# Kernel tuning notes

Hardware: AMD Instinct MI355X
Metric: run time of the kernel (lower is better)

Reference implementation:

```python
import jax, jax.numpy as jnp
import numpy as np

N_NODES = 50000


def _gcn_conv(x, src, dst, W, b, n_nodes):
    # x: [N, Fin] -> h: [N, Fout]; GCN: D^-1/2 (A+I) D^-1/2 (x W) + b
    h = x @ W
    deg = jax.ops.segment_sum(jnp.ones_like(dst, dtype=h.dtype), dst,
                              num_segments=n_nodes)
    dinv = jax.lax.rsqrt(jnp.maximum(deg, 1.0))
    norm = dinv[src] * dinv[dst]                      # [E]
    msg = h[src] * norm[:, None]                      # [E, Fout] gather
    agg = jax.ops.segment_sum(msg, dst, num_segments=n_nodes)  # scatter-add
    return agg + b


def setup_inputs() -> dict:
    key = jax.random.key(0)
    k0, k1, k2, k3 = jax.random.split(key, 4)
    N, E, F_IN, H, C = N_NODES, 800000, 128, 128, 16
    x = jax.random.normal(k0, (N, F_IN), dtype=jnp.float32)
    edge_index = jax.random.randint(k1, (2, E), 0, N, dtype=jnp.int64)
    W1 = jax.random.normal(k2, (F_IN, H), dtype=jnp.float32) / np.sqrt(F_IN)
    b1 = jnp.zeros((H,), dtype=jnp.float32)
    W2 = jax.random.normal(k3, (H, C), dtype=jnp.float32) / np.sqrt(H)
    b2 = jnp.zeros((C,), dtype=jnp.float32)
    return {"x": x, "edge_index": edge_index, "W1": W1, "b1": b1,
            "W2": W2, "b2": b2}


def reference(x, edge_index, W1, b1, W2, b2):
    n = x.shape[0]
    # add self-loops (shared by both conv layers)
    loops = jnp.arange(n, dtype=edge_index.dtype)
    src = jnp.concatenate([edge_index[0], loops])
    dst = jnp.concatenate([edge_index[1], loops])
    h = _gcn_conv(x, src, dst, W1, b1, n)
    h = jax.nn.relu(h)
    # dropout p=0.5 is identity in eval mode
    h = _gcn_conv(h, src, dst, W2, b2, n)
    return jax.nn.log_softmax(h, axis=1)
```

## Files before the change

kernel.cpp:

```cpp
#include <hip/hip_runtime.h>
#include <hip/hip_fp16.h>
#include <math.h>


#define NBUCKET_SHIFT 8
#define BIN_CHUNK 4096
#define PAD_SLOP (7 << NBUCKET_SHIFT)
#define CAP  5120
#define CCAP (CAP + PAD_SLOP)

typedef __bf16 bf16x8 __attribute__((ext_vector_type(8)));
typedef float  f32x4  __attribute__((ext_vector_type(4)));
typedef float  f32x2  __attribute__((ext_vector_type(2)));

__device__ __forceinline__ unsigned short pack_bf16(float f) {
    unsigned u = __float_as_uint(f);
    return (unsigned short)((u + 0x7fffu + ((u >> 16) & 1u)) >> 16);
}

__device__ __forceinline__ float unpack_w(unsigned u) {
    return __half2float(__ushort_as_half((unsigned short)(u >> 16)));
}

__device__ __forceinline__ void acc_fp8x16_fma(f32x2* a, uint4 v, float w) {
    f32x2 ww; ww.x = w; ww.y = w;
    a[0] += __builtin_amdgcn_cvt_pk_f32_fp8(v.x, false) * ww;
    a[1] += __builtin_amdgcn_cvt_pk_f32_fp8(v.x, true)  * ww;
    a[2] += __builtin_amdgcn_cvt_pk_f32_fp8(v.y, false) * ww;
    a[3] += __builtin_amdgcn_cvt_pk_f32_fp8(v.y, true)  * ww;
    a[4] += __builtin_amdgcn_cvt_pk_f32_fp8(v.z, false) * ww;
    a[5] += __builtin_amdgcn_cvt_pk_f32_fp8(v.z, true)  * ww;
    a[6] += __builtin_amdgcn_cvt_pk_f32_fp8(v.w, false) * ww;
    a[7] += __builtin_amdgcn_cvt_pk_f32_fp8(v.w, true)  * ww;
}

__device__ __forceinline__ void acc_fp16x8(f32x2* a, uint4 v) {
    float2 f;
    f = __half22float2(*(const __half2*)&v.x); a[0] += *(f32x2*)&f;
    f = __half22float2(*(const __half2*)&v.y); a[1] += *(f32x2*)&f;
    f = __half22float2(*(const __half2*)&v.z); a[2] += *(f32x2*)&f;
    f = __half22float2(*(const __half2*)&v.w); a[3] += *(f32x2*)&f;
}

union K1Smem {
    struct { unsigned spair[BIN_CHUNK]; int lcnt[256]; int lbase[256]; } b;
    unsigned short wtp[16384];
    float outb[4][16 * 132];
};

__global__ __launch_bounds__(256)
void bin_gemm1_kernel(const int* __restrict__ src, const int* __restrict__ dst,
                      int* __restrict__ bcur, unsigned* __restrict__ pairs,
                      int* __restrict__ deg, int E, int nbuckets, int nbins,
                      const float* __restrict__ x, const float* __restrict__ W1,
                      unsigned* __restrict__ h1b, int N) {
    __shared__ K1Smem sm;
    const int blk = blockIdx.x;
    const int tid = threadIdx.x;

    if (blk < nbins) {
        const int e0 = blk * BIN_CHUNK;
        const int cnt = min(BIN_CHUNK, E - e0);
        sm.b.lcnt[tid] = 0;
        __syncthreads();
        for (int i = tid; i < cnt; i += 256) {
            unsigned s = (unsigned)src[e0 + i], d = (unsigned)dst[e0 + i];
            sm.b.spair[i] = (d >> NBUCKET_SHIFT) << 24 | (d & 255u) << 16 | s;
            atomicAdd(&sm.b.lcnt[d >> NBUCKET_SHIFT], 1);
            atomicAdd(&deg[d], 1);
        }
        __syncthreads();
        if (tid < nbuckets) {
            int c = sm.b.lcnt[tid];
            sm.b.lbase[tid] = (c > 0) ? atomicAdd(&bcur[tid], c) : 0;
            sm.b.lcnt[tid] = 0;
        }
        __syncthreads();
        for (int i = tid; i < cnt; i += 256) {
            unsigned p = sm.b.spair[i];
            int b = (int)(p >> 24);
            int off = atomicAdd(&sm.b.lcnt[b], 1);
            pairs[b * CAP + sm.b.lbase[b] + off] = p;
        }
        return;
    }

    const int gblk = blk - nbins;
    const int wave = tid >> 6, lane = tid & 63;
    const int q = lane >> 4, m = lane & 15;
    const int row0 = gblk * 64 + wave * 16;
    const int row = row0 + m;
    const int rowc = (row < N) ? row : (N - 1);

    for (int it = tid; it < 16384; it += 256) {
        int k = it >> 7, n = it & 127;
        int t = n >> 4, mm = n & 15;
        int ks = k >> 5;
        int lane2 = (((k & 31) >> 3) << 4) | mm;
        int j = k & 7;
        sm.wtp[(t * 4 + ks) * 512 + lane2 * 8 + j] = pack_bf16(W1[it]);
    }
    __syncthreads();

    f32x4 acc[8];
#pragma unroll
    for (int t = 0; t < 8; t++) acc[t] = (f32x4)0.0f;

#pragma unroll
    for (int ks = 0; ks < 4; ks++) {
        const float4* xp = (const float4*)(x + (size_t)rowc * 128 + ks * 32 + q * 8);
        float4 f0 = xp[0], f1 = xp[1];
        float fv[8] = {f0.x, f0.y, f0.z, f0.w, f1.x, f1.y, f1.z, f1.w};
        bf16x8 ah;
#pragma unroll
        for (int j = 0; j < 8; j++) ah[j] = (__bf16)fv[j];
#pragma unroll
        for (int t = 0; t < 8; t++) {
            bf16x8 b = *(const bf16x8*)(sm.wtp + (size_t)(t * 4 + ks) * 512 + lane * 8);
            acc[t] = __builtin_amdgcn_mfma_f32_16x16x32_bf16(ah, b, acc[t], 0, 0, 0);
        }
    }
    __syncthreads();

#pragma unroll
    for (int t = 0; t < 8; t++)
#pragma unroll
        for (int r = 0; r < 4; r++)
            sm.outb[wave][(q * 4 + r) * 132 + t * 16 + m] = acc[t][r];
    __syncthreads();

    const int r2 = lane >> 2, j = lane & 3;
    const int orow = row0 + r2;
    if (orow < N) {
        const float* lrow = &sm.outb[wave][r2 * 132];
#pragma unroll
        for (int s = 0; s < 4; s++) {
            float4 a = *(const float4*)(lrow + s * 32 + j * 8);
            float4 b = *(const float4*)(lrow + s * 32 + j * 8 + 4);
            unsigned lo = __builtin_amdgcn_cvt_pk_fp8_f32(a.x, a.y, 0, false);
            lo = __builtin_amdgcn_cvt_pk_fp8_f32(a.z, a.w, lo, true);
            unsigned hi = __builtin_amdgcn_cvt_pk_fp8_f32(b.x, b.y, 0, false);
            hi = __builtin_amdgcn_cvt_pk_fp8_f32(b.z, b.w, hi, true);
            ((uint2*)h1b)[((size_t)(s >> 1) * (N + 1) + orow) * 8 + (s & 1) * 4 + j]
                = make_uint2(lo, hi);
        }
    }
}

__global__ __launch_bounds__(256)
void bucket_build_kernel(const int* __restrict__ bcur, const unsigned* __restrict__ pairs,
                         const int* __restrict__ deg,
                         int* __restrict__ rowptr, int* __restrict__ rowcnt,
                         float* __restrict__ dinv, unsigned* __restrict__ colsrc,
                         unsigned* __restrict__ h1b, int N, int nbuckets) {
    __shared__ int cnt[256];
    __shared__ int sm[256];
    const int tid = threadIdx.x;
    const int blk = blockIdx.x;
    const int nb0 = blk << NBUCKET_SHIFT;

    if (blk == 0) {
        if (tid < 16) h1b[((size_t)0 * (N + 1) + N) * 16 + tid] = 0u;
        else if (tid < 32) h1b[((size_t)1 * (N + 1) + N) * 16 + (tid - 16)] = 0u;
        else if (tid == 32) dinv[N] = 0.0f;
    }

    const int lo = blk * CAP;
    const int hi = lo + bcur[blk];

    int node = nb0 + tid;
    int v = (node < N) ? deg[node] : 0;
    int pdeg = (v + 7) & ~7;
    sm[tid] = pdeg;
    __syncthreads();
#pragma unroll
    for (int off = 1; off < 256; off <<= 1) {
        int u = (tid >= off) ? sm[tid - off] : 0;
        __syncthreads();
        sm[tid] += u;
        __syncthreads();
    }
    int pexcl = sm[tid] - pdeg;
    const int start = blk * CCAP + pexcl;
    if (node < N) {
        rowptr[node] = start;
        rowcnt[node] = pdeg;
        dinv[node] = rsqrtf((float)v + 1.0f);
    }
    __syncthreads();
    cnt[tid] = start;
    __syncthreads();
    for (int i = lo + tid; i < hi; i += 256) {
        unsigned p = pairs[i];
        unsigned s = p & 0xffffu;
        int pos = atomicAdd(&cnt[(int)(p >> 16) & 255], 1);
        float w = rsqrtf((float)deg[s] + 1.0f);
        unsigned w16 = (unsigned)__half_as_ushort(__float2half_rn(w));
        colsrc[pos] = s | (w16 << 16);
    }
    for (int p = start + v; p < start + pdeg; ++p)
        colsrc[p] = (unsigned)N;
}

__global__ __launch_bounds__(256)
void l1_fused_kernel(const int* __restrict__ rowptr, const int* __restrict__ rowcnt,
                     const unsigned* __restrict__ colsrc,
                     const float* __restrict__ dinv, const unsigned* __restrict__ h1b,
                     const float* __restrict__ b1, const float* __restrict__ W2,
                     float* __restrict__ h2acc, int N) {
    __shared__ float rows[4][4][68];
    __shared__ float w2s[64 * 16];
    const int tid = threadIdx.x;
    const int wave = tid >> 6, lane = tid & 63;
    const int c = lane & 3;
    const int g = (lane >> 2) & 3;
    const int n = lane >> 4;
    const int p = blockIdx.x & 1;
    const int d = (blockIdx.x >> 1) * 16 + wave * 4 + n;

    for (int i = tid; i < 256; i += 256)
        ((float4*)w2s)[i] = ((const float4*)W2)[p * 256 + i];

    const uint4* hq = (const uint4*)h1b + (size_t)p * (N + 1) * 4;

    if (d < N) {
        const float dvd = dinv[d];
        f32x2 a[8];
#pragma unroll
        for (int j = 0; j < 8; j++) a[j] = (f32x2)0.0f;

        if (g == 0)
            acc_fp8x16_fma(a, hq[(size_t)d * 4 + c], dvd);

        int i = rowptr[d];
        const int end = i + rowcnt[d];
        unsigned u0 = 0, u1 = 0, u2 = 0, u3 = 0;
        if (i + 16 <= end) {
            u0 = colsrc[i + g];      u1 = colsrc[i + g + 4];
            u2 = colsrc[i + g + 8];  u3 = colsrc[i + g + 12];
        }
        while (i + 16 <= end) {
            uint4 v0 = hq[(size_t)(u0 & 0xffffu) * 4 + c];
            uint4 v1 = hq[(size_t)(u1 & 0xffffu) * 4 + c];
            uint4 v2 = hq[(size_t)(u2 & 0xffffu) * 4 + c];
            uint4 v3 = hq[(size_t)(u3 & 0xffffu) * 4 + c];
            float w0 = unpack_w(u0), w1 = unpack_w(u1);
            float w2 = unpack_w(u2), w3 = unpack_w(u3);
            i += 16;
            if (i + 16 <= end) {
                u0 = colsrc[i + g];      u1 = colsrc[i + g + 4];
                u2 = colsrc[i + g + 8];  u3 = colsrc[i + g + 12];
            }
            acc_fp8x16_fma(a, v0, w0); acc_fp8x16_fma(a, v1, w1);
            acc_fp8x16_fma(a, v2, w2); acc_fp8x16_fma(a, v3, w3);
        }
        for (; i + 4 <= end; i += 4) {
            unsigned ux = colsrc[i + g];
            acc_fp8x16_fma(a, hq[(size_t)(ux & 0xffffu) * 4 + c], unpack_w(ux));
        }

#pragma unroll
        for (int j = 0; j < 8; j++) {
            a[j].x += __shfl_xor(a[j].x, 4, 64);
            a[j].y += __shfl_xor(a[j].y, 4, 64);
            a[j].x += __shfl_xor(a[j].x, 8, 64);
            a[j].y += __shfl_xor(a[j].y, 8, 64);
        }

        if (g == 0) {
            float* rbase = &rows[wave][n][c * 16];
#pragma unroll
            for (int t = 0; t < 4; t++) {
                float4 bb = ((const float4*)b1)[p * 16 + c * 4 + t];
                float4 o;
                o.x = fmaxf(a[2 * t].x * dvd + bb.x, 0.0f);
                o.y = fmaxf(a[2 * t].y * dvd + bb.y, 0.0f);
                o.z = fmaxf(a[2 * t + 1].x * dvd + bb.z, 0.0f);
                o.w = fmaxf(a[2 * t + 1].y * dvd + bb.w, 0.0f);
                *(float4*)(rbase + 4 * t) = o;
            }
        }
    }
    __syncthreads();

    const int n2 = lane >> 4, col = lane & 15;
    const int d2 = (blockIdx.x >> 1) * 16 + wave * 4 + n2;
    if (d2 < N) {
        const float* r = &rows[wave][n2][0];
        float p0 = 0.0f, p1 = 0.0f;
#pragma unroll
        for (int k = 0; k < 32; k++) {
            p0 = fmaf(r[k],      w2s[k * 16 + col],        p0);
            p1 = fmaf(r[k + 32], w2s[(k + 32) * 16 + col], p1);
        }
        atomicAdd(&h2acc[(size_t)d2 * 16 + col], p0 + p1);
    }
}

__global__ __launch_bounds__(256)
void h2cvt_kernel(const float* __restrict__ h2acc, const float* __restrict__ dinv,
                  unsigned* __restrict__ h2h, int N) {
    int idx = blockIdx.x * 256 + threadIdx.x;
    if (idx >= (N + 1) * 4) return;
    float dv = dinv[idx >> 2];
    float4 v = ((const float4*)h2acc)[idx];
    __half2 lo = __floats2half2_rn(v.x * dv, v.y * dv);
    __half2 hi = __floats2half2_rn(v.z * dv, v.w * dv);
    ((uint2*)h2h)[idx] = make_uint2(*(unsigned*)&lo, *(unsigned*)&hi);
}

__global__ __launch_bounds__(256)
void l2_kernel(const int* __restrict__ rowptr, const int* __restrict__ rowcnt,
               const unsigned* __restrict__ colsrc,
               const float* __restrict__ dinv, const unsigned* __restrict__ h2s,
               const float* __restrict__ b2, float* __restrict__ out, int N) {
    const int tid = threadIdx.x;
    const int wave = tid >> 6, lane = tid & 63;
    const int n = lane >> 4;
    const int g = (lane >> 1) & 7;
    const int c = lane & 1;
    const int d = blockIdx.x * 16 + wave * 4 + n;
    if (d >= N) return;
    const uint4* h2q = (const uint4*)h2s;

    f32x2 a[4];
#pragma unroll
    for (int j = 0; j < 4; j++) a[j] = (f32x2)0.0f;

    if (g == 0)
        acc_fp16x8(a, h2q[(size_t)d * 2 + c]);

    int i = rowptr[d];
    const int end = i + rowcnt[d];
    uint4 v; unsigned u2 = 0;
    if (i < end) {
        unsigned u = colsrc[i + g];
        v = h2q[(size_t)(u & 0xffffu) * 2 + c];
    }
    if (i + 8 < end) u2 = colsrc[i + 8 + g];
    while (i < end) {
        uint4 vc = v;
        if (i + 8 < end) v = h2q[(size_t)(u2 & 0xffffu) * 2 + c];
        if (i + 16 < end) u2 = colsrc[i + 16 + g];
        i += 8;
        acc_fp16x8(a, vc);
    }

#pragma unroll
    for (int j = 0; j < 4; j++) {
#pragma unroll
        for (int off = 2; off <= 8; off <<= 1) {
            a[j].x += __shfl_xor(a[j].x, off, 64);
            a[j].y += __shfl_xor(a[j].y, off, 64);
        }
    }

    const float dv = dinv[d];
    const float* af = (const float*)a;
    float v8[8];
#pragma unroll
    for (int j = 0; j < 8; j++) v8[j] = af[j] * dv + b2[c * 8 + j];

    float m = v8[0];
#pragma unroll
    for (int j = 1; j < 8; j++) m = fmaxf(m, v8[j]);
    m = fmaxf(m, __shfl_xor(m, 1, 64));
    float e = 0.0f;
#pragma unroll
    for (int j = 0; j < 8; j++) e += expf(v8[j] - m);
    e += __shfl_xor(e, 1, 64);
    float lse = m + logf(e);

    if (g == 0) {
        float4 o0 = make_float4(v8[0] - lse, v8[1] - lse, v8[2] - lse, v8[3] - lse);
        float4 o1 = make_float4(v8[4] - lse, v8[5] - lse, v8[6] - lse, v8[7] - lse);
        float4* op = (float4*)(out + (size_t)d * 16 + c * 8);
        op[0] = o0; op[1] = o1;
    }
}

extern "C" void kernel_launch(void* const* d_in, const int* in_sizes, int n_in,
                              void* d_out, int out_size, void* d_ws, size_t ws_size,
                              hipStream_t stream) {
    const float* x  = (const float*)d_in[0];
    const int*  ei  = (const int*)d_in[1];
    const float* W1 = (const float*)d_in[2];
    const float* b1 = (const float*)d_in[3];
    const float* W2 = (const float*)d_in[4];
    const float* b2 = (const float*)d_in[5];
    float* out = (float*)d_out;

    const int N = in_sizes[0] / 128;
    const int E = in_sizes[1] / 2;
    const int* src = ei;
    const int* dst = ei + E;
    const int nbuckets = (N + 255) >> NBUCKET_SHIFT;
    const int nbins = (E + BIN_CHUNK - 1) / BIN_CHUNK;
    const int g1blocks = (N + 63) / 64;

    float*          wsf     = (float*)d_ws;
    float*          dinv    = wsf;
    int*            rowptr  = (int*)(wsf + N + 16);
    int*            rowcnt  = rowptr + N;
    int*            bcur    = rowcnt + N;
    int*            deg     = bcur + 256;
    float*          h2acc   = (float*)(deg + N + 16);
    unsigned*       colsrc  = (unsigned*)(h2acc + (size_t)(N + 1) * 16);
    unsigned*       pairs   = colsrc + (size_t)nbuckets * CCAP;
    unsigned*       h1b     = pairs + (size_t)nbuckets * CAP;
    unsigned*       h2h     = pairs;

    const size_t zero_ints = 256 + (size_t)(N + 16) + (size_t)(N + 1) * 16;

    hipMemsetAsync(bcur, 0, zero_ints * sizeof(int), stream);
    bin_gemm1_kernel<<<nbins + g1blocks, 256, 0, stream>>>(src, dst, bcur, pairs,
                                                           deg, E, nbuckets, nbins,
                                                           x, W1, h1b, N);

    bucket_build_kernel<<<nbuckets, 256, 0, stream>>>(bcur, pairs, deg, rowptr,
                                                      rowcnt, dinv, colsrc, h1b,
                                                      N, nbuckets);

    l1_fused_kernel<<<((N + 15) / 16) * 2, 256, 0, stream>>>(rowptr, rowcnt, colsrc,
                                                             dinv, h1b, b1, W2,
                                                             h2acc, N);

    h2cvt_kernel<<<((N + 1) * 4 + 255) / 256, 256, 0, stream>>>(h2acc, dinv, h2h, N);

    l2_kernel<<<(N + 15) / 16, 256, 0, stream>>>(rowptr, rowcnt, colsrc, dinv, h2h,
                                                 b2, out, N);
}
```

Measured before the change: 181.3 us.

## Compute degrees per bucket in LDS and pack edge weights in a separate pass

Removes the global atomicAdd on deg[] from the binning kernel and instead counts in-degree per destination with LDS atomics inside bucket_build, since each bucket already holds all pairs for its 256 nodes. Because a source node's degree is not known until every bucket finishes, the fp16 dinv weight packing moves into a new pack_kernel that runs after bucket_build and reads a dinv16 array. This trades about 800k global atomics, and a deg array that had to be zeroed, for an extra kernel launch and an extra read-modify-write pass over colsrc.

```diff
diff --git a/kernel.cpp b/kernel.cpp
--- a/kernel.cpp
+++ b/kernel.cpp
@@ -8,6 +8,7 @@
 #define PAD_SLOP (7 << NBUCKET_SHIFT)
 #define CAP  5120
 #define CCAP (CAP + PAD_SLOP)
+#define PSTRIPES 8
 
 typedef __bf16 bf16x8 __attribute__((ext_vector_type(8)));
 typedef float  f32x4  __attribute__((ext_vector_type(4)));
@@ -51,7 +52,7 @@
 __global__ __launch_bounds__(256)
 void bin_gemm1_kernel(const int* __restrict__ src, const int* __restrict__ dst,
                       int* __restrict__ bcur, unsigned* __restrict__ pairs,
-                      int* __restrict__ deg, int E, int nbuckets, int nbins,
+                      int E, int nbuckets, int nbins,
                       const float* __restrict__ x, const float* __restrict__ W1,
                       unsigned* __restrict__ h1b, int N) {
     __shared__ K1Smem sm;
@@ -67,7 +68,6 @@
             unsigned s = (unsigned)src[e0 + i], d = (unsigned)dst[e0 + i];
             sm.b.spair[i] = (d >> NBUCKET_SHIFT) << 24 | (d & 255u) << 16 | s;
             atomicAdd(&sm.b.lcnt[d >> NBUCKET_SHIFT], 1);
-            atomicAdd(&deg[d], 1);
         }
         __syncthreads();
         if (tid < nbuckets) {
@@ -149,9 +149,9 @@
 
 __global__ __launch_bounds__(256)
 void bucket_build_kernel(const int* __restrict__ bcur, const unsigned* __restrict__ pairs,
-                         const int* __restrict__ deg,
                          int* __restrict__ rowptr, int* __restrict__ rowcnt,
-                         float* __restrict__ dinv, unsigned* __restrict__ colsrc,
+                         float* __restrict__ dinv, unsigned short* __restrict__ dinv16,
+                         int* __restrict__ ptot, unsigned* __restrict__ colsrc,
                          unsigned* __restrict__ h1b, int N, int nbuckets) {
     __shared__ int cnt[256];
     __shared__ int sm[256];
@@ -162,14 +162,19 @@
     if (blk == 0) {
         if (tid < 16) h1b[((size_t)0 * (N + 1) + N) * 16 + tid] = 0u;
         else if (tid < 32) h1b[((size_t)1 * (N + 1) + N) * 16 + (tid - 16)] = 0u;
-        else if (tid == 32) dinv[N] = 0.0f;
+        else if (tid == 32) { dinv[N] = 0.0f; dinv16[N] = 0; }
     }
 
     const int lo = blk * CAP;
     const int hi = lo + bcur[blk];
-
-    int node = nb0 + tid;
-    int v = (node < N) ? deg[node] : 0;
+    cnt[tid] = 0;
+    __syncthreads();
+
+    for (int i = lo + tid; i < hi; i += 256)
+        atomicAdd(&cnt[(int)(pairs[i] >> 16) & 255], 1);
+    __syncthreads();
+
+    int v = cnt[tid];
     int pdeg = (v + 7) & ~7;
     sm[tid] = pdeg;
     __syncthreads();
@@ -182,24 +187,38 @@
     }
     int pexcl = sm[tid] - pdeg;
     const int start = blk * CCAP + pexcl;
+    int node = nb0 + tid;
     if (node < N) {
         rowptr[node] = start;
         rowcnt[node] = pdeg;
-        dinv[node] = rsqrtf((float)v + 1.0f);
-    }
+        float w = rsqrtf((float)v + 1.0f);
+        dinv[node] = w;
+        dinv16[node] = __half_as_ushort(__float2half_rn(w));
+    }
+    if (tid == 255) ptot[blk] = sm[255];
     __syncthreads();
     cnt[tid] = start;
     __syncthreads();
     for (int i = lo + tid; i < hi; i += 256) {
         unsigned p = pairs[i];
-        unsigned s = p & 0xffffu;
         int pos = atomicAdd(&cnt[(int)(p >> 16) & 255], 1);
-        float w = rsqrtf((float)deg[s] + 1.0f);
-        unsigned w16 = (unsigned)__half_as_ushort(__float2half_rn(w));
-        colsrc[pos] = s | (w16 << 16);
+        colsrc[pos] = p & 0xffffu;
     }
     for (int p = start + v; p < start + pdeg; ++p)
         colsrc[p] = (unsigned)N;
+}
+
+__global__ __launch_bounds__(256)
+void pack_kernel(const int* __restrict__ ptot, const unsigned short* __restrict__ dinv16,
+                 unsigned* __restrict__ colsrc, int nbuckets) {
+    const int bkt = blockIdx.x / PSTRIPES;
+    const int st  = blockIdx.x % PSTRIPES;
+    const int tot = ptot[bkt];
+    const size_t base = (size_t)bkt * CCAP;
+    for (int i = st * 256 + threadIdx.x; i < tot; i += 256 * PSTRIPES) {
+        unsigned u = colsrc[base + i];
+        colsrc[base + i] = u | ((unsigned)dinv16[u] << 16);
+    }
 }
 
 __global__ __launch_bounds__(256)
@@ -403,23 +422,25 @@
     int*            rowptr  = (int*)(wsf + N + 16);
     int*            rowcnt  = rowptr + N;
     int*            bcur    = rowcnt + N;
-    int*            deg     = bcur + 256;
-    float*          h2acc   = (float*)(deg + N + 16);
-    unsigned*       colsrc  = (unsigned*)(h2acc + (size_t)(N + 1) * 16);
+    float*          h2acc   = (float*)(bcur + 256);
+    int*            ptot    = (int*)(h2acc + (size_t)(N + 1) * 16);
+    unsigned short* dinv16  = (unsigned short*)(ptot + 256);
+    unsigned*       colsrc  = (unsigned*)(ptot + 256 + (N + 16) / 2);
     unsigned*       pairs   = colsrc + (size_t)nbuckets * CCAP;
     unsigned*       h1b     = pairs + (size_t)nbuckets * CAP;
     unsigned*       h2h     = pairs;
 
-    const size_t zero_ints = 256 + (size_t)(N + 16) + (size_t)(N + 1) * 16;
-
-    hipMemsetAsync(bcur, 0, zero_ints * sizeof(int), stream);
+    hipMemsetAsync(bcur, 0, (256 + (size_t)(N + 1) * 16) * sizeof(int), stream);
     bin_gemm1_kernel<<<nbins + g1blocks, 256, 0, stream>>>(src, dst, bcur, pairs,
-                                                           deg, E, nbuckets, nbins,
+                                                           E, nbuckets, nbins,
                                                            x, W1, h1b, N);
 
-    bucket_build_kernel<<<nbuckets, 256, 0, stream>>>(bcur, pairs, deg, rowptr,
-                                                      rowcnt, dinv, colsrc, h1b,
-                                                      N, nbuckets);
+    bucket_build_kernel<<<nbuckets, 256, 0, stream>>>(bcur, pairs, rowptr, rowcnt,
+                                                      dinv, dinv16, ptot, colsrc,
+                                                      h1b, N, nbuckets);
+
+    pack_kernel<<<nbuckets * PSTRIPES, 256, 0, stream>>>(ptot, dinv16, colsrc,
+                                                         nbuckets);
 
     l1_fused_kernel<<<((N + 15) / 16) * 2, 256, 0, stream>>>(rowptr, rowcnt, colsrc,
                                                              dinv, h1b, b1, W2,
```

Result: faster. 165.3 us (-8.8%).
